# Optimization experiments

Measured on AMD Instinct MI355X. Metric: run time of the kernel, lower is better.

The kernel has to match this reference:

```python
import jax, jax.numpy as jnp
import numpy as np

B, S, DIM = 2, 2048, 2048
NH, NKV = 16, 8
HD = DIM // NH  # 128
ROPE_THETA = 10000.0


def setup_inputs() -> dict:
    key = jax.random.key(0)
    ks = jax.random.split(key, 7)
    std = DIM ** -0.5
    x = jax.random.normal(ks[0], (B, S, DIM), jnp.float32)
    wq = jax.random.normal(ks[1], (NH * HD, DIM), jnp.float32) * std
    wk = jax.random.normal(ks[2], (NKV * HD, DIM), jnp.float32) * std
    wv = jax.random.normal(ks[3], (NKV * HD, DIM), jnp.float32) * std
    wo = jax.random.normal(ks[4], (DIM, NH * HD), jnp.float32) * std
    inv_freq = 1.0 / (ROPE_THETA ** (jnp.arange(0, HD, 2, dtype=jnp.float32) / HD))
    ang = jnp.arange(S, dtype=jnp.float32)[:, None] * inv_freq[None, :]  # [S, HD//2]
    freqs_cos = jnp.cos(ang)
    freqs_sin = jnp.sin(ang)
    # diffusion-style random per-batch token mask: t ~ U[0,1) per batch row
    t = jax.random.uniform(ks[5], (B, 1))
    mask = jax.random.uniform(ks[6], (B, S)) < t  # True = masked key
    mask = mask.at[:, 0].set(False)  # first token never masked
    return dict(x=x, wq=wq, wk=wk, wv=wv, wo=wo,
                freqs_cos=freqs_cos, freqs_sin=freqs_sin, mask=mask)


def _rope(x, cos, sin):
    # x: [b, s, h, d]; pairs (x[2i], x[2i+1]) rotated by angle[s, i]
    xr, xi = x[..., 0::2], x[..., 1::2]
    c = cos[None, :, None, :]
    s = sin[None, :, None, :]
    out = jnp.stack([xr * c - xi * s, xr * s + xi * c], axis=-1)
    return out.reshape(x.shape)


def reference(x, wq, wk, wv, wo, freqs_cos, freqs_sin, mask):
    b, s, _ = x.shape
    xq = jnp.einsum('bsd,ed->bse', x, wq).reshape(b, s, NH, HD)
    xk = jnp.einsum('bsd,ed->bse', x, wk).reshape(b, s, NKV, HD)
    xv = jnp.einsum('bsd,ed->bse', x, wv).reshape(b, s, NKV, HD)
    xq = _rope(xq, freqs_cos, freqs_sin)
    xk = _rope(xk, freqs_cos, freqs_sin)
    n_rep = NH // NKV
    xk = jnp.repeat(xk, n_rep, axis=2)  # repeat_kv (GQA)
    xv = jnp.repeat(xv, n_rep, axis=2)
    q = xq.transpose(0, 2, 1, 3)  # [b, h, s, d]
    k = xk.transpose(0, 2, 1, 3)
    v = xv.transpose(0, 2, 1, 3)
    scale = 1.0 / np.sqrt(HD).astype(np.float32)
    scores = jnp.einsum('bhqd,bhkd->bhqk', q, k) * scale  # [b, h, s, s]
    scores = jnp.where(mask[:, None, None, :], -jnp.inf, scores)
    probs = jax.nn.softmax(scores, axis=-1)
    out = jnp.einsum('bhqk,bhkd->bhqd', probs, v)
    out = out.transpose(0, 2, 1, 3).reshape(b, s, NH * HD)
    return jnp.einsum('bse,de->bsd', out, wo)
```

## Files before the change

kernel.cpp:

```cpp
#include <hip/hip_runtime.h>
#include <hip/hip_bf16.h>
#include <cstdint>
#include <cstddef>

#define S_LEN   2048
#define NHQ     16
#define NKV_H   8
#define HD_DIM  128
#define DMODEL  2048
#define BATCH   2
#define KVD     (NKV_H * HD_DIM)

typedef float f32x4  __attribute__((ext_vector_type(4)));
typedef __bf16 bf16x8 __attribute__((ext_vector_type(8)));

__device__ __forceinline__ void gload_lds16(const __bf16* g, __bf16* l) {
    __builtin_amdgcn_global_load_lds(
        (const __attribute__((address_space(1))) void*)g,
        (__attribute__((address_space(3))) void*)l, 16, 0, 0);
}

__global__ void sniff_x_kernel(const unsigned* __restrict__ x,
                               int* __restrict__ flag) {
    __shared__ int cnt;
    if (threadIdx.x == 0) cnt = 0;
    __syncthreads();
    int c = 0;
    for (int j = threadIdx.x; j < 1024; j += 256) {
        unsigned hw = x[j] & 0xFFFFu;
        unsigned e  = (hw >> 7) & 0xFF;
        if (hw == 0u || (e >= 118 && e <= 132)) c++;
    }
    atomicAdd(&cnt, c);
    __syncthreads();
    if (threadIdx.x == 0) *flag = (cnt > 512) ? 1 : 0;
}

__global__ void sniff_fc_kernel(const unsigned* __restrict__ fc,
                                int* __restrict__ flag) {
    if (threadIdx.x == 0) *flag = (fc[0] == 0x3F803F80u) ? 1 : 0;
}

__global__ void mask_norm_kernel(const unsigned char* __restrict__ mraw,
                                 unsigned char* __restrict__ mout, int n) {
    __shared__ int f_bf16, f_f32, f_u8;
    if (threadIdx.x == 0) { f_bf16 = 0; f_f32 = 0; f_u8 = 0; }
    __syncthreads();
    const unsigned* dw = (const unsigned*)mraw;
    int ndw = n / 4;
    for (int j = threadIdx.x; j < ndw; j += blockDim.x) {
        unsigned v = dw[j];
        if (v == 0x00003F80u || v == 0x3F803F80u) f_bf16 = 1;
        else if (v == 0x3F800000u) f_f32 = 1;
        else if (v & 0xFFFFFFFEu) f_u8 = 1;
    }
    __syncthreads();
    int layout;
    if (f_bf16) layout = 3;
    else if (f_f32) layout = 2;
    else if (f_u8) layout = 0;
    else layout = 1;
    for (int i = threadIdx.x; i < n; i += blockDim.x) {
        unsigned v;
        if (layout == 0)      v = mraw[i];
        else if (layout == 3) v = ((const unsigned short*)mraw)[i];
        else                  v = ((const unsigned*)mraw)[i];
        mout[i] = v ? 1u : 0u;
    }
}

__global__ __launch_bounds__(256)
void conv_bf16_kernel(const void* __restrict__ src, __bf16* __restrict__ dst,
                      int n8, const int* __restrict__ dflag) {
    int i = blockIdx.x * blockDim.x + threadIdx.x;
    if (i >= n8) return;
    size_t off = (size_t)i * 8;
    if (*dflag) {
        *reinterpret_cast<uint4*>(dst + off) =
            *reinterpret_cast<const uint4*>((const __bf16*)src + off);
    } else {
        const float* f = (const float*)src + off;
        float4 a = *reinterpret_cast<const float4*>(f);
        float4 b = *reinterpret_cast<const float4*>(f + 4);
        bf16x8 v;
        v[0] = (__bf16)a.x; v[1] = (__bf16)a.y; v[2] = (__bf16)a.z; v[3] = (__bf16)a.w;
        v[4] = (__bf16)b.x; v[5] = (__bf16)b.y; v[6] = (__bf16)b.z; v[7] = (__bf16)b.w;
        *reinterpret_cast<bf16x8*>(dst + off) = v;
    }
}

template <bool OUT_BF16>
__global__ __launch_bounds__(256)
void gemm_bt_async(const __bf16* __restrict__ A, const __bf16* __restrict__ Bw,
                   void* __restrict__ Cv, int M, int N, int K) {
    __shared__ __align__(16) __bf16 As[128 * 64];
    __shared__ __align__(16) __bf16 Bs[128 * 64];

    const int t    = threadIdx.x;
    const int w    = t >> 6;
    const int lane = t & 63;
    const int quad = lane >> 4;
    const int l16  = lane & 15;
    const int wm   = (w >> 1) * 64;
    const int wn   = (w & 1) * 64;
    const int m0   = blockIdx.x * 128;
    const int n0   = blockIdx.y * 128;
    const int rl   = lane >> 3;
    const int gl   = lane & 7;

    f32x4 acc[4][4];
#pragma unroll
    for (int i = 0; i < 4; ++i)
#pragma unroll
        for (int j = 0; j < 4; ++j) acc[i][j] = (f32x4){0.f, 0.f, 0.f, 0.f};

    for (int k0 = 0; k0 < K; k0 += 64) {
        __syncthreads();
#pragma unroll
        for (int p = 0; p < 4; ++p) {
            const int rowb = w * 32 + p * 8;
            const int r    = rowb + rl;
            const int gA   = gl ^ rl;
            gload_lds16(A  + (size_t)(m0 + r) * K + k0 + gA * 8, &As[rowb * 64]);
            gload_lds16(Bw + (size_t)(n0 + r) * K + k0 + gA * 8, &Bs[rowb * 64]);
        }
        __syncthreads();
#pragma unroll
        for (int ks = 0; ks < 2; ++ks) {
            const int G = ks * 4 + quad;
            const int gsw = (G ^ (l16 & 7)) * 8;
            bf16x8 af[4], bf[4];
#pragma unroll
            for (int i = 0; i < 4; ++i)
                af[i] = *reinterpret_cast<const bf16x8*>(
                    &As[(wm + i * 16 + l16) * 64 + gsw]);
#pragma unroll
            for (int j = 0; j < 4; ++j)
                bf[j] = *reinterpret_cast<const bf16x8*>(
                    &Bs[(wn + j * 16 + l16) * 64 + gsw]);
#pragma unroll
            for (int i = 0; i < 4; ++i)
#pragma unroll
                for (int j = 0; j < 4; ++j)
                    acc[i][j] = __builtin_amdgcn_mfma_f32_16x16x32_bf16(
                        af[i], bf[j], acc[i][j], 0, 0, 0);
        }
    }
#pragma unroll
    for (int i = 0; i < 4; ++i)
#pragma unroll
        for (int r = 0; r < 4; ++r) {
            size_t m = (size_t)(m0 + wm + i * 16 + quad * 4 + r);
#pragma unroll
            for (int j = 0; j < 4; ++j) {
                int n = n0 + wn + j * 16 + l16;
                if constexpr (OUT_BF16)
                    ((__hip_bfloat16*)Cv)[m * N + n] = __float2bfloat16(acc[i][j][r]);
                else
                    ((float*)Cv)[m * N + n] = acc[i][j][r];
            }
        }
}

__global__ void rope_kernel(__hip_bfloat16* __restrict__ xqk,
                            const void* __restrict__ cosv,
                            const void* __restrict__ sinv,
                            const int* __restrict__ dflag_fc,
                            int nheads, int npairs) {
    int idx = blockIdx.x * blockDim.x + threadIdx.x;
    if (idx >= npairs) return;
    int i  = idx & 63;
    int h  = (idx >> 6) % nheads;
    int bs = idx / (64 * nheads);
    int s  = bs & (S_LEN - 1);
    float c, sn;
    if (*dflag_fc) {
        c  = __bfloat162float(((const __hip_bfloat16*)cosv)[s * 64 + i]);
        sn = __bfloat162float(((const __hip_bfloat16*)sinv)[s * 64 + i]);
    } else {
        c  = ((const float*)cosv)[s * 64 + i];
        sn = ((const float*)sinv)[s * 64 + i];
    }
    unsigned* p = (unsigned*)(xqk + (size_t)bs * (nheads * HD_DIM) + h * HD_DIM) + i;
    unsigned u = *p;
    float xr = __uint_as_float(u << 16);
    float xi = __uint_as_float(u & 0xFFFF0000u);
    float o0 = xr * c - xi * sn;
    float o1 = xr * sn + xi * c;
    union { __hip_bfloat16 h2[2]; unsigned u32; } out;
    out.h2[0] = __float2bfloat16(o0);
    out.h2[1] = __float2bfloat16(o1);
    *p = out.u32;
}

__global__ __launch_bounds__(256)
void transpose_v_kernel(const __hip_bfloat16* __restrict__ xv,
                        __hip_bfloat16* __restrict__ vt) {
    __shared__ unsigned short T[32][36];
    const int t  = threadIdx.x;
    const int s0 = blockIdx.x * 32;
    const int d0 = blockIdx.y * 32;
    const int z  = blockIdx.z;
    const int b  = z >> 3;
    const int kv = z & 7;
    {
        int sr = t >> 3, dc = (t & 7) * 4;
        const unsigned short* p = (const unsigned short*)xv
            + (size_t)(b * S_LEN + s0 + sr) * KVD + kv * 128 + d0 + dc;
        uint2 v = *reinterpret_cast<const uint2*>(p);
        T[sr][dc + 0] = (unsigned short)(v.x & 0xFFFFu);
        T[sr][dc + 1] = (unsigned short)(v.x >> 16);
        T[sr][dc + 2] = (unsigned short)(v.y & 0xFFFFu);
        T[sr][dc + 3] = (unsigned short)(v.y >> 16);
    }
    __syncthreads();
    {
        int dr = t >> 3, sc = (t & 7) * 4;
        unsigned w0 = (unsigned)T[sc + 0][dr] | ((unsigned)T[sc + 1][dr] << 16);
        unsigned w1 = (unsigned)T[sc + 2][dr] | ((unsigned)T[sc + 3][dr] << 16);
        unsigned short* q = (unsigned short*)vt
            + ((size_t)z * 128 + d0 + dr) * S_LEN + s0 + sc;
        uint2 v; v.x = w0; v.y = w1;
        *reinterpret_cast<uint2*>(q) = v;
    }
}

__global__ __launch_bounds__(256)
void attn_mfma2_kernel(const __hip_bfloat16* xq,
                       const __hip_bfloat16* __restrict__ xk,
                       const __hip_bfloat16* __restrict__ vt_g,
                       const unsigned char* __restrict__ msk,
                       __hip_bfloat16* att) {
    __shared__ __align__(16) __bf16 Ks[64 * 128];
    __shared__ __align__(16) __bf16 Vt[128 * 64];
    __shared__ __align__(16) __bf16 Ps[4][16][64];

    const int t    = threadIdx.x;
    const int w    = t >> 6;
    const int lane = t & 63;
    const int quad = lane >> 4;
    const int l16  = lane & 15;

    const int bid = blockIdx.x;
    const int qt  = bid & 31;
    const int h   = (bid >> 5) & (NHQ - 1);
    const int b   = bid >> 9;
    const int kvh = h >> 1;
    const int q0  = qt * 64;

    bf16x8 qf[4];
    {
        const __bf16* qrow = (const __bf16*)xq
            + (size_t)(b * S_LEN + q0 + w * 16 + l16) * DMODEL + h * 128 + quad * 8;
#pragma unroll
        for (int ks = 0; ks < 4; ++ks)
            qf[ks] = *reinterpret_cast<const bf16x8*>(qrow + ks * 32);
    }

    float m_r[4], l_r[4];
    f32x4 o[8];
#pragma unroll
    for (int r = 0; r < 4; ++r) { m_r[r] = -INFINITY; l_r[r] = 0.f; }
#pragma unroll
    for (int d0 = 0; d0 < 8; ++d0) o[d0] = (f32x4){0.f, 0.f, 0.f, 0.f};

    const float scale2 = 0.08838834764831845f * 1.4426950408889634f;

    const int krl = lane >> 4, kgl = lane & 15;
    const int vrl = lane >> 3, vgl = lane & 7;

    for (int k0 = 0; k0 < S_LEN; k0 += 64) {
        __syncthreads();
#pragma unroll
        for (int p = 0; p < 4; ++p) {
            const int row  = w * 16 + p * 4 + krl;
            const int srcg = kgl ^ (row & 7);
            gload_lds16((const __bf16*)xk + (size_t)(b * S_LEN + k0 + row) * KVD
                            + kvh * 128 + srcg * 8,
                        &Ks[(w * 16 + p * 4) * 128]);
        }
#pragma unroll
        for (int p = 0; p < 4; ++p) {
            const int row  = w * 32 + p * 8 + vrl;
            const int srcg = vgl ^ (row & 7);
            gload_lds16((const __bf16*)vt_g
                            + ((size_t)(b * NKV_H + kvh) * 128 + row) * S_LEN
                            + k0 + srcg * 8,
                        &Vt[(w * 32 + p * 8) * 64]);
        }
        int mk[4];
#pragma unroll
        for (int n0 = 0; n0 < 4; ++n0)
            mk[n0] = msk[b * S_LEN + k0 + n0 * 16 + l16];
        __syncthreads();

        f32x4 sc4[4];
#pragma unroll
        for (int n0 = 0; n0 < 4; ++n0) sc4[n0] = (f32x4){0.f, 0.f, 0.f, 0.f};
#pragma unroll
        for (int ks = 0; ks < 4; ++ks) {
            const int G = ks * 4 + quad;
#pragma unroll
            for (int n0 = 0; n0 < 4; ++n0) {
                const int row  = n0 * 16 + l16;
                const int slot = G ^ (row & 7);
                bf16x8 bf = *reinterpret_cast<const bf16x8*>(&Ks[row * 128 + slot * 8]);
                sc4[n0] = __builtin_amdgcn_mfma_f32_16x16x32_bf16(qf[ks], bf, sc4[n0], 0, 0, 0);
            }
        }

#pragma unroll
        for (int n0 = 0; n0 < 4; ++n0)
#pragma unroll
            for (int r = 0; r < 4; ++r) {
                float v = sc4[n0][r] * scale2;
                sc4[n0][r] = mk[n0] ? -INFINITY : v;
            }
        float alpha[4];
#pragma unroll
        for (int r = 0; r < 4; ++r) {
            float rmax = fmaxf(fmaxf(sc4[0][r], sc4[1][r]), fmaxf(sc4[2][r], sc4[3][r]));
#pragma unroll
            for (int m = 1; m < 16; m <<= 1)
                rmax = fmaxf(rmax, __shfl_xor(rmax, m, 64));
            float mn = fmaxf(m_r[r], rmax);
            alpha[r] = exp2f(m_r[r] - mn);
            m_r[r] = mn;
            float rs = 0.f;
#pragma unroll
            for (int n0 = 0; n0 < 4; ++n0) {
                float p = exp2f(sc4[n0][r] - mn);
                sc4[n0][r] = p;
                rs += p;
            }
#pragma unroll
            for (int m = 1; m < 16; m <<= 1)
                rs += __shfl_xor(rs, m, 64);
            l_r[r] = l_r[r] * alpha[r] + rs;
        }
#pragma unroll
        for (int d0 = 0; d0 < 8; ++d0)
#pragma unroll
            for (int r = 0; r < 4; ++r) o[d0][r] *= alpha[r];

#pragma unroll
        for (int n0 = 0; n0 < 4; ++n0) {
            const int G = n0 * 2 + (l16 >> 3);
            const int cs = l16 & 7;
#pragma unroll
            for (int r = 0; r < 4; ++r) {
                const int row  = quad * 4 + r;
                const int slot = G ^ (row & 7);
                Ps[w][row][slot * 8 + cs] = (__bf16)sc4[n0][r];
            }
        }

#pragma unroll
        for (int kk = 0; kk < 64; kk += 32) {
            const int Gp    = (kk >> 3) + quad;
            const int slotp = Gp ^ (l16 & 7);
            bf16x8 af = *reinterpret_cast<const bf16x8*>(&Ps[w][l16][slotp * 8]);
#pragma unroll
            for (int d0 = 0; d0 < 8; ++d0) {
                const int row  = d0 * 16 + l16;
                const int slot = Gp ^ (row & 7);
                bf16x8 bf = *reinterpret_cast<const bf16x8*>(&Vt[row * 64 + slot * 8]);
                o[d0] = __builtin_amdgcn_mfma_f32_16x16x32_bf16(af, bf, o[d0], 0, 0, 0);
            }
        }
    }

    float inv[4];
#pragma unroll
    for (int r = 0; r < 4; ++r) inv[r] = 1.f / l_r[r];
#pragma unroll
    for (int d0 = 0; d0 < 8; ++d0)
#pragma unroll
        for (int r = 0; r < 4; ++r) {
            size_t row = (size_t)(b * S_LEN + q0 + w * 16 + quad * 4 + r);
            att[row * DMODEL + h * 128 + d0 * 16 + l16] =
                __float2bfloat16(o[d0][r] * inv[r]);
        }
}

extern "C" void kernel_launch(void* const* d_in, const int* in_sizes, int n_in,
                              void* d_out, int out_size, void* d_ws, size_t ws_size,
                              hipStream_t stream) {
    const void* x  = d_in[0];
    const void* wq = d_in[1];
    const void* wk = d_in[2];
    const void* wv = d_in[3];
    const void* wo = d_in[4];
    const void* fc = d_in[5];
    const void* fs = d_in[6];
    const unsigned char* mraw = (const unsigned char*)d_in[7];

    const int M = BATCH * S_LEN;
    char* wsb = (char*)d_ws;
    int* dflag_x  = (int*)wsb;
    int* dflag_fc = (int*)(wsb + 64);
    unsigned char* mnorm = (unsigned char*)(wsb + 128);
    __hip_bfloat16* xq = (__hip_bfloat16*)(wsb + 8192);
    __hip_bfloat16* xk = xq + (size_t)M * DMODEL;
    __hip_bfloat16* xv = xk + (size_t)M * KVD;
    __hip_bfloat16* att = xq;
    __hip_bfloat16* wob = xk;

    char* dob = (char*)d_out;
    __bf16* xb  = (__bf16*)dob;
    __bf16* wqb = (__bf16*)(dob + (16u << 20));
    __bf16* wkb = (__bf16*)(dob + (24u << 20));
    __bf16* wvb = (__bf16*)(dob + (28u << 20));
    __hip_bfloat16* vt = (__hip_bfloat16*)d_out;

    hipLaunchKernelGGL(sniff_x_kernel, dim3(1), dim3(256), 0, stream,
                       (const unsigned*)x, dflag_x);
    hipLaunchKernelGGL(sniff_fc_kernel, dim3(1), dim3(64), 0, stream,
                       (const unsigned*)fc, dflag_fc);
    hipLaunchKernelGGL(mask_norm_kernel, dim3(1), dim3(256), 0, stream,
                       mraw, mnorm, BATCH * S_LEN);

    hipLaunchKernelGGL(conv_bf16_kernel, dim3((M * DMODEL / 8) / 256), dim3(256), 0, stream,
                       x, xb, M * DMODEL / 8, dflag_x);
    hipLaunchKernelGGL(conv_bf16_kernel, dim3((DMODEL * DMODEL / 8) / 256), dim3(256), 0, stream,
                       wq, wqb, DMODEL * DMODEL / 8, dflag_x);
    hipLaunchKernelGGL(conv_bf16_kernel, dim3((KVD * DMODEL / 8) / 256), dim3(256), 0, stream,
                       wk, wkb, KVD * DMODEL / 8, dflag_x);
    hipLaunchKernelGGL(conv_bf16_kernel, dim3((KVD * DMODEL / 8) / 256), dim3(256), 0, stream,
                       wv, wvb, KVD * DMODEL / 8, dflag_x);

    hipLaunchKernelGGL((gemm_bt_async<true>), dim3(M / 128, DMODEL / 128), dim3(256), 0, stream,
                       xb, wqb, (void*)xq, M, DMODEL, DMODEL);
    hipLaunchKernelGGL((gemm_bt_async<true>), dim3(M / 128, KVD / 128), dim3(256), 0, stream,
                       xb, wkb, (void*)xk, M, KVD, DMODEL);
    hipLaunchKernelGGL((gemm_bt_async<true>), dim3(M / 128, KVD / 128), dim3(256), 0, stream,
                       xb, wvb, (void*)xv, M, KVD, DMODEL);

    int npq = M * NHQ * (HD_DIM / 2);
    int npk = M * NKV_H * (HD_DIM / 2);
    hipLaunchKernelGGL(rope_kernel, dim3(npq / 256), dim3(256), 0, stream,
                       xq, fc, fs, dflag_fc, NHQ, npq);
    hipLaunchKernelGGL(rope_kernel, dim3(npk / 256), dim3(256), 0, stream,
                       xk, fc, fs, dflag_fc, NKV_H, npk);

    hipLaunchKernelGGL(transpose_v_kernel, dim3(S_LEN / 32, HD_DIM / 32, BATCH * NKV_H),
                       dim3(256), 0, stream, xv, vt);

    hipLaunchKernelGGL(attn_mfma2_kernel, dim3(BATCH * NHQ * (S_LEN / 64)), dim3(256), 0, stream,
                       xq, xk, vt, mnorm, att);

    hipLaunchKernelGGL(conv_bf16_kernel, dim3((DMODEL * DMODEL / 8) / 256), dim3(256), 0, stream,
                       wo, (__bf16*)wob, DMODEL * DMODEL / 8, dflag_x);
    hipLaunchKernelGGL((gemm_bt_async<false>), dim3(M / 128, DMODEL / 128), dim3(256), 0, stream,
                       (const __bf16*)att, (const __bf16*)wob, d_out, M, DMODEL, DMODEL);
}
```

Measured before the change: 526.6 us.

## Fuse QKV projections into one GEMM, merge RoPE, add lazy softmax rescale

The three Q/K/V projection GEMMs become a single GEMM over concatenated weights, writing into a combined QKV buffer with row stride 4096. The two RoPE launches are merged into one. Attention now skips the running-max rescale unless the max grows by more than a threshold, defers the row-sum shuffle reduction to the end, and raises wave priority around the MFMA sections. The output weight is converted into the strided buffer, removing launches and per-iteration reductions at the cost of more complex indexing and softmax ranges that rely on the threshold bound.

```diff
diff --git a/kernel.cpp b/kernel.cpp
--- a/kernel.cpp
+++ b/kernel.cpp
@@ -10,6 +10,7 @@
 #define DMODEL  2048
 #define BATCH   2
 #define KVD     (NKV_H * HD_DIM)
+#define QKV_LD  4096
 
 typedef float f32x4  __attribute__((ext_vector_type(4)));
 typedef __bf16 bf16x8 __attribute__((ext_vector_type(8)));
@@ -89,10 +90,34 @@
     }
 }
 
+__global__ __launch_bounds__(256)
+void conv_bf16_strided_kernel(const void* __restrict__ src,
+                              __bf16* __restrict__ dstbase,
+                              int n8, const int* __restrict__ dflag) {
+    int i = blockIdx.x * blockDim.x + threadIdx.x;
+    if (i >= n8) return;
+    size_t off = (size_t)i * 8;
+    size_t row = off >> 11;
+    size_t col = off & 2047;
+    __bf16* dst = dstbase + row * QKV_LD + col;
+    if (*dflag) {
+        *reinterpret_cast<uint4*>(dst) =
+            *reinterpret_cast<const uint4*>((const __bf16*)src + off);
+    } else {
+        const float* f = (const float*)src + off;
+        float4 a = *reinterpret_cast<const float4*>(f);
+        float4 b = *reinterpret_cast<const float4*>(f + 4);
+        bf16x8 v;
+        v[0] = (__bf16)a.x; v[1] = (__bf16)a.y; v[2] = (__bf16)a.z; v[3] = (__bf16)a.w;
+        v[4] = (__bf16)b.x; v[5] = (__bf16)b.y; v[6] = (__bf16)b.z; v[7] = (__bf16)b.w;
+        *reinterpret_cast<bf16x8*>(dst) = v;
+    }
+}
+
 template <bool OUT_BF16>
 __global__ __launch_bounds__(256)
 void gemm_bt_async(const __bf16* __restrict__ A, const __bf16* __restrict__ Bw,
-                   void* __restrict__ Cv, int M, int N, int K) {
+                   void* __restrict__ Cv, int K, int lda, int ldb, int ldc) {
     __shared__ __align__(16) __bf16 As[128 * 64];
     __shared__ __align__(16) __bf16 Bs[128 * 64];
 
@@ -121,8 +146,8 @@
             const int rowb = w * 32 + p * 8;
             const int r    = rowb + rl;
             const int gA   = gl ^ rl;
-            gload_lds16(A  + (size_t)(m0 + r) * K + k0 + gA * 8, &As[rowb * 64]);
-            gload_lds16(Bw + (size_t)(n0 + r) * K + k0 + gA * 8, &Bs[rowb * 64]);
+            gload_lds16(A  + (size_t)(m0 + r) * lda + k0 + gA * 8, &As[rowb * 64]);
+            gload_lds16(Bw + (size_t)(n0 + r) * ldb + k0 + gA * 8, &Bs[rowb * 64]);
         }
         __syncthreads();
 #pragma unroll
@@ -155,9 +180,9 @@
             for (int j = 0; j < 4; ++j) {
                 int n = n0 + wn + j * 16 + l16;
                 if constexpr (OUT_BF16)
-                    ((__hip_bfloat16*)Cv)[m * N + n] = __float2bfloat16(acc[i][j][r]);
+                    ((__hip_bfloat16*)Cv)[m * ldc + n] = __float2bfloat16(acc[i][j][r]);
                 else
-                    ((float*)Cv)[m * N + n] = acc[i][j][r];
+                    ((float*)Cv)[m * ldc + n] = acc[i][j][r];
             }
         }
 }
@@ -166,12 +191,12 @@
                             const void* __restrict__ cosv,
                             const void* __restrict__ sinv,
                             const int* __restrict__ dflag_fc,
-                            int nheads, int npairs) {
+                            int npairs) {
     int idx = blockIdx.x * blockDim.x + threadIdx.x;
     if (idx >= npairs) return;
     int i  = idx & 63;
-    int h  = (idx >> 6) % nheads;
-    int bs = idx / (64 * nheads);
+    int h  = (idx >> 6) % 24;
+    int bs = idx / (64 * 24);
     int s  = bs & (S_LEN - 1);
     float c, sn;
     if (*dflag_fc) {
@@ -181,7 +206,7 @@
         c  = ((const float*)cosv)[s * 64 + i];
         sn = ((const float*)sinv)[s * 64 + i];
     }
-    unsigned* p = (unsigned*)(xqk + (size_t)bs * (nheads * HD_DIM) + h * HD_DIM) + i;
+    unsigned* p = (unsigned*)(xqk + (size_t)bs * QKV_LD + h * HD_DIM) + i;
     unsigned u = *p;
     float xr = __uint_as_float(u << 16);
     float xi = __uint_as_float(u & 0xFFFF0000u);
@@ -206,7 +231,7 @@
     {
         int sr = t >> 3, dc = (t & 7) * 4;
         const unsigned short* p = (const unsigned short*)xv
-            + (size_t)(b * S_LEN + s0 + sr) * KVD + kv * 128 + d0 + dc;
+            + (size_t)(b * S_LEN + s0 + sr) * QKV_LD + kv * 128 + d0 + dc;
         uint2 v = *reinterpret_cast<const uint2*>(p);
         T[sr][dc + 0] = (unsigned short)(v.x & 0xFFFFu);
         T[sr][dc + 1] = (unsigned short)(v.x >> 16);
@@ -226,11 +251,9 @@
 }
 
 __global__ __launch_bounds__(256)
-void attn_mfma2_kernel(const __hip_bfloat16* xq,
-                       const __hip_bfloat16* __restrict__ xk,
+void attn_mfma2_kernel(__hip_bfloat16* qkv,
                        const __hip_bfloat16* __restrict__ vt_g,
-                       const unsigned char* __restrict__ msk,
-                       __hip_bfloat16* att) {
+                       const unsigned char* __restrict__ msk) {
     __shared__ __align__(16) __bf16 Ks[64 * 128];
     __shared__ __align__(16) __bf16 Vt[128 * 64];
     __shared__ __align__(16) __bf16 Ps[4][16][64];
@@ -250,8 +273,8 @@
 
     bf16x8 qf[4];
     {
-        const __bf16* qrow = (const __bf16*)xq
-            + (size_t)(b * S_LEN + q0 + w * 16 + l16) * DMODEL + h * 128 + quad * 8;
+        const __bf16* qrow = (const __bf16*)qkv
+            + (size_t)(b * S_LEN + q0 + w * 16 + l16) * QKV_LD + h * 128 + quad * 8;
 #pragma unroll
         for (int ks = 0; ks < 4; ++ks)
             qf[ks] = *reinterpret_cast<const bf16x8*>(qrow + ks * 32);
@@ -265,6 +288,8 @@
     for (int d0 = 0; d0 < 8; ++d0) o[d0] = (f32x4){0.f, 0.f, 0.f, 0.f};
 
     const float scale2 = 0.08838834764831845f * 1.4426950408889634f;
+
+    const __bf16* xk = (const __bf16*)qkv + 2048;
 
     const int krl = lane >> 4, kgl = lane & 15;
     const int vrl = lane >> 3, vgl = lane & 7;
@@ -275,7 +300,7 @@
         for (int p = 0; p < 4; ++p) {
             const int row  = w * 16 + p * 4 + krl;
             const int srcg = kgl ^ (row & 7);
-            gload_lds16((const __bf16*)xk + (size_t)(b * S_LEN + k0 + row) * KVD
+            gload_lds16(xk + (size_t)(b * S_LEN + k0 + row) * QKV_LD
                             + kvh * 128 + srcg * 8,
                         &Ks[(w * 16 + p * 4) * 128]);
         }
@@ -297,6 +322,7 @@
         f32x4 sc4[4];
 #pragma unroll
         for (int n0 = 0; n0 < 4; ++n0) sc4[n0] = (f32x4){0.f, 0.f, 0.f, 0.f};
+        __builtin_amdgcn_s_setprio(1);
 #pragma unroll
         for (int ks = 0; ks < 4; ++ks) {
             const int G = ks * 4 + quad;
@@ -308,40 +334,50 @@
                 sc4[n0] = __builtin_amdgcn_mfma_f32_16x16x32_bf16(qf[ks], bf, sc4[n0], 0, 0, 0);
             }
         }
+        __builtin_amdgcn_s_setprio(0);
 
 #pragma unroll
         for (int n0 = 0; n0 < 4; ++n0)
 #pragma unroll
+            for (int r = 0; r < 4; ++r)
+                sc4[n0][r] = mk[n0] ? -INFINITY : sc4[n0][r];
+
+        float tmax[4];
+#pragma unroll
+        for (int r = 0; r < 4; ++r) {
+            float rm = fmaxf(fmaxf(sc4[0][r], sc4[1][r]), fmaxf(sc4[2][r], sc4[3][r]));
+#pragma unroll
+            for (int m = 1; m < 16; m <<= 1)
+                rm = fmaxf(rm, __shfl_xor(rm, m, 64));
+            tmax[r] = rm;
+        }
+
+        bool need = false;
+#pragma unroll
+        for (int r = 0; r < 4; ++r)
+            need = need || ((tmax[r] - m_r[r]) * scale2 > 8.0f);
+        if (__any((int)need)) {
+#pragma unroll
             for (int r = 0; r < 4; ++r) {
-                float v = sc4[n0][r] * scale2;
-                sc4[n0][r] = mk[n0] ? -INFINITY : v;
-            }
-        float alpha[4];
+                float mn = fmaxf(m_r[r], tmax[r]);
+                float al = exp2f((m_r[r] - mn) * scale2);
+                m_r[r] = mn;
+                l_r[r] *= al;
+#pragma unroll
+                for (int d0 = 0; d0 < 8; ++d0) o[d0][r] *= al;
+            }
+        }
+
 #pragma unroll
         for (int r = 0; r < 4; ++r) {
-            float rmax = fmaxf(fmaxf(sc4[0][r], sc4[1][r]), fmaxf(sc4[2][r], sc4[3][r]));
-#pragma unroll
-            for (int m = 1; m < 16; m <<= 1)
-                rmax = fmaxf(rmax, __shfl_xor(rmax, m, 64));
-            float mn = fmaxf(m_r[r], rmax);
-            alpha[r] = exp2f(m_r[r] - mn);
-            m_r[r] = mn;
-            float rs = 0.f;
+            float negm = -m_r[r] * scale2;
 #pragma unroll
             for (int n0 = 0; n0 < 4; ++n0) {
-                float p = exp2f(sc4[n0][r] - mn);
+                float p = exp2f(fmaf(sc4[n0][r], scale2, negm));
                 sc4[n0][r] = p;
-                rs += p;
-            }
-#pragma unroll
-            for (int m = 1; m < 16; m <<= 1)
-                rs += __shfl_xor(rs, m, 64);
-            l_r[r] = l_r[r] * alpha[r] + rs;
-        }
-#pragma unroll
-        for (int d0 = 0; d0 < 8; ++d0)
-#pragma unroll
-            for (int r = 0; r < 4; ++r) o[d0][r] *= alpha[r];
+                l_r[r] += p;
+            }
+        }
 
 #pragma unroll
         for (int n0 = 0; n0 < 4; ++n0) {
@@ -355,6 +391,7 @@
             }
         }
 
+        __builtin_amdgcn_s_setprio(1);
 #pragma unroll
         for (int kk = 0; kk < 64; kk += 32) {
             const int Gp    = (kk >> 3) + quad;
@@ -368,17 +405,25 @@
                 o[d0] = __builtin_amdgcn_mfma_f32_16x16x32_bf16(af, bf, o[d0], 0, 0, 0);
             }
         }
+        __builtin_amdgcn_s_setprio(0);
     }
 
     float inv[4];
 #pragma unroll
-    for (int r = 0; r < 4; ++r) inv[r] = 1.f / l_r[r];
+    for (int r = 0; r < 4; ++r) {
+        float ls = l_r[r];
+#pragma unroll
+        for (int m = 1; m < 16; m <<= 1)
+            ls += __shfl_xor(ls, m, 64);
+        inv[r] = 1.f / ls;
+    }
+    __hip_bfloat16* att = qkv;
 #pragma unroll
     for (int d0 = 0; d0 < 8; ++d0)
 #pragma unroll
         for (int r = 0; r < 4; ++r) {
             size_t row = (size_t)(b * S_LEN + q0 + w * 16 + quad * 4 + r);
-            att[row * DMODEL + h * 128 + d0 * 16 + l16] =
+            att[row * QKV_LD + h * 128 + d0 * 16 + l16] =
                 __float2bfloat16(o[d0][r] * inv[r]);
         }
 }
@@ -400,17 +445,14 @@
     int* dflag_x  = (int*)wsb;
     int* dflag_fc = (int*)(wsb + 64);
     unsigned char* mnorm = (unsigned char*)(wsb + 128);
-    __hip_bfloat16* xq = (__hip_bfloat16*)(wsb + 8192);
-    __hip_bfloat16* xk = xq + (size_t)M * DMODEL;
-    __hip_bfloat16* xv = xk + (size_t)M * KVD;
-    __hip_bfloat16* att = xq;
-    __hip_bfloat16* wob = xk;
+    __hip_bfloat16* qkv = (__hip_bfloat16*)(wsb + 8192);
 
     char* dob = (char*)d_out;
-    __bf16* xb  = (__bf16*)dob;
-    __bf16* wqb = (__bf16*)(dob + (16u << 20));
-    __bf16* wkb = (__bf16*)(dob + (24u << 20));
-    __bf16* wvb = (__bf16*)(dob + (28u << 20));
+    __bf16* xb    = (__bf16*)dob;
+    __bf16* wcomb = (__bf16*)(dob + (16u << 20));
+    __bf16* wqb = wcomb;
+    __bf16* wkb = wcomb + (size_t)2048 * 2048;
+    __bf16* wvb = wcomb + (size_t)3072 * 2048;
     __hip_bfloat16* vt = (__hip_bfloat16*)d_out;
 
     hipLaunchKernelGGL(sniff_x_kernel, dim3(1), dim3(256), 0, stream,
@@ -429,28 +471,23 @@
     hipLaunchKernelGGL(conv_bf16_kernel, dim3((KVD * DMODEL / 8) / 256), dim3(256), 0, stream,
                        wv, wvb, KVD * DMODEL / 8, dflag_x);
 
-    hipLaunchKernelGGL((gemm_bt_async<true>), dim3(M / 128, DMODEL / 128), dim3(256), 0, stream,
-                       xb, wqb, (void*)xq, M, DMODEL, DMODEL);
-    hipLaunchKernelGGL((gemm_bt_async<true>), dim3(M / 128, KVD / 128), dim3(256), 0, stream,
-                       xb, wkb, (void*)xk, M, KVD, DMODEL);
-    hipLaunchKernelGGL((gemm_bt_async<true>), dim3(M / 128, KVD / 128), dim3(256), 0, stream,
-                       xb, wvb, (void*)xv, M, KVD, DMODEL);
-
-    int npq = M * NHQ * (HD_DIM / 2);
-    int npk = M * NKV_H * (HD_DIM / 2);
-    hipLaunchKernelGGL(rope_kernel, dim3(npq / 256), dim3(256), 0, stream,
-                       xq, fc, fs, dflag_fc, NHQ, npq);
-    hipLaunchKernelGGL(rope_kernel, dim3(npk / 256), dim3(256), 0, stream,
-                       xk, fc, fs, dflag_fc, NKV_H, npk);
+    hipLaunchKernelGGL((gemm_bt_async<true>), dim3(M / 128, QKV_LD / 128), dim3(256), 0, stream,
+                       xb, wcomb, (void*)qkv, DMODEL, DMODEL, DMODEL, QKV_LD);
+
+    int npairs = M * 24 * (HD_DIM / 2);
+    hipLaunchKernelGGL(rope_kernel, dim3(npairs / 256), dim3(256), 0, stream,
+                       qkv, fc, fs, dflag_fc, npairs);
 
     hipLaunchKernelGGL(transpose_v_kernel, dim3(S_LEN / 32, HD_DIM / 32, BATCH * NKV_H),
-                       dim3(256), 0, stream, xv, vt);
+                       dim3(256), 0, stream, qkv + 3072, vt);
 
     hipLaunchKernelGGL(attn_mfma2_kernel, dim3(BATCH * NHQ * (S_LEN / 64)), dim3(256), 0, stream,
-                       xq, xk, vt, mnorm, att);
-
-    hipLaunchKernelGGL(conv_bf16_kernel, dim3((DMODEL * DMODEL / 8) / 256), dim3(256), 0, stream,
-                       wo, (__bf16*)wob, DMODEL * DMODEL / 8, dflag_x);
+                       qkv, vt, mnorm);
+
+    hipLaunchKernelGGL(conv_bf16_strided_kernel, dim3((DMODEL * DMODEL / 8) / 256), dim3(256), 0, stream,
+                       wo, (__bf16*)qkv + 2048, DMODEL * DMODEL / 8, dflag_x);
+
     hipLaunchKernelGGL((gemm_bt_async<false>), dim3(M / 128, DMODEL / 128), dim3(256), 0, stream,
-                       (const __bf16*)att, (const __bf16*)wob, d_out, M, DMODEL, DMODEL);
-}
+                       (const __bf16*)qkv, (const __bf16*)qkv + 2048, d_out,
+                       DMODEL, QKV_LD, QKV_LD, DMODEL);
+}
```

After: 460.3 us. 12.6% less time.
